# Optimization experiments

Measured on AMD Instinct MI355X. Metric: run time of the kernel, lower is better.

The kernel has to match this reference:

```python
import jax, jax.numpy as jnp
import numpy as np

STRIDES = (2, 2, 2, 2)
ALPHA = 1.0
NEG_SLOPE = 0.1


def _conv1d(h, w, b, stride):
    # h: (N, C, L), w: (O, I, K) -> (N, O, L_out), VALID padding
    out = jax.lax.conv_general_dilated(
        h, w, window_strides=(stride,), padding='VALID',
        dimension_numbers=('NCH', 'OIH', 'NCH'))
    return out + b[None, :, None]


def setup_inputs() -> dict:
    key = jax.random.key(0)
    ks = jax.random.split(key, 10)
    N, C, L = 256, 128, 1024
    k_sizes = (15, 12, 7, 4)
    inp = {'x': jax.random.normal(ks[0], (N, C, L), dtype=jnp.float32)}
    for i, k in enumerate(k_sizes):
        fan_in = C * k
        scale = 1.0 / np.sqrt(fan_in).astype(np.float32)
        inp[f'w{i+1}'] = jax.random.normal(ks[1 + 2 * i], (C, C, k), dtype=jnp.float32) * scale
        inp[f'b{i+1}'] = jax.random.normal(ks[2 + 2 * i], (C,), dtype=jnp.float32) * 0.01
    D = C * 59  # flattened encoder output: 1024->505->247->121->59
    inp['centers'] = jax.random.normal(ks[9], (64, D), dtype=jnp.float32)
    return inp


def reference(x, w1, b1, w2, b2, w3, b3, w4, b4, centers):
    ws = [(w1, b1), (w2, b2), (w3, b3), (w4, b4)]
    h = x
    for i, ((w, b), s) in enumerate(zip(ws, STRIDES)):
        h = _conv1d(h, w, b, s)
        if i != len(ws) - 1:
            h = jnp.where(h > 0, h, NEG_SLOPE * h)  # LeakyReLU(0.1)
    z = h.reshape(h.shape[0], -1)  # (N, D)
    # squared distances via norm expansion: ||z||^2 + ||c||^2 - 2 z.c
    d2 = (jnp.sum(z * z, axis=1, keepdims=True)
          + jnp.sum(centers * centers, axis=1)[None, :]
          - 2.0 * z @ centers.T)  # (N, K)
    q = 1.0 / (1.0 + d2 / ALPHA)
    q = q ** ((ALPHA + 1.0) / 2.0)
    q = q / jnp.sum(q, axis=1, keepdims=True)
    return q
```

## Files before the change

### kernel.cpp

```cpp
#include <hip/hip_runtime.h>

typedef __bf16 bf16;
typedef __bf16 bf16x4 __attribute__((ext_vector_type(4)));
typedef __bf16 bf16x8 __attribute__((ext_vector_type(8)));
typedef float f32x4 __attribute__((ext_vector_type(4)));

#define CCH 128

__global__ void k_prep_wall(const float* __restrict__ w1, const float* __restrict__ w2,
                            const float* __restrict__ w3, const float* __restrict__ w4,
                            bf16* __restrict__ o1, bf16* __restrict__ o2,
                            bf16* __restrict__ o3, bf16* __restrict__ o4) {
    int idx = blockIdx.x * 256 + threadIdx.x;
    const float* src; bf16* dst; int Kw; int r = idx;
    if (r < 15 * 16384) { src = w1; dst = o1; Kw = 15; }
    else if ((r -= 15 * 16384) < 12 * 16384) { src = w2; dst = o2; Kw = 12; }
    else if ((r -= 12 * 16384) < 7 * 16384) { src = w3; dst = o3; Kw = 7; }
    else if ((r -= 7 * 16384) < 4 * 16384) { src = w4; dst = o4; Kw = 4; }
    else return;
    int e = r & 7, lane = (r >> 3) & 63, og = (r >> 9) & 7, c = (r >> 12) & 3, kt = r >> 14;
    int o = og * 16 + (lane & 15);
    int i = c * 32 + (lane >> 4) * 8 + e;
    dst[r] = (bf16)src[(o * 128 + i) * Kw + kt];
}

__global__ void k_prep_c(const float* __restrict__ c, bf16* __restrict__ cbp,
                         float* __restrict__ cc) {
    int k = blockIdx.x;
    int tid = threadIdx.x;
    float s = 0.f;
    for (int idx = tid; idx < 64 * 128; idx += 256) {
        int l = idx >> 7;
        int o = idx & 127;
        float v = (l < 59) ? c[k * 7552 + o * 59 + l] : 0.f;
        bf16 b = (bf16)v;
        cbp[(size_t)k * 64 * 128 + idx] = b;
        float fv = (float)b;
        s += fv * fv;
    }
    __shared__ float red[256];
    red[tid] = s;
    __syncthreads();
    for (int st = 128; st > 0; st >>= 1) {
        if (tid < st) red[tid] += red[tid + st];
        __syncthreads();
    }
    if (tid == 0) cc[k] = red[0];
}

__global__ __launch_bounds__(256, 4) void k_conv1(
    const float* __restrict__ x, const bf16* __restrict__ wTp,
    const float* __restrict__ bias, bf16* __restrict__ out) {
    constexpr int KW = 15, LT = 128, PH = 2, OUT_ROWS = 512;
    constexpr int P = (LT - 1) * 2 + KW;
    constexpr int CPP = 64;
    constexpr int KC = 2;
    constexpr int RS = CPP;
    constexpr int NLT = LT / 16;
    constexpr int ESE = 136;
    constexpr int SMELE = (P * RS > LT * ESE) ? P * RS : LT * ESE;
    constexpr int NJ = KW * KC;
    __shared__ __align__(16) bf16 smem[SMELE];

    const int n = blockIdx.y;
    const int l0 = blockIdx.x * LT;
    const int p0 = l0 * 2;
    const int tid = threadIdx.x;
    const int wid = tid >> 6;
    const int lane = tid & 63;
    const int quad = lane >> 4;
    const int l15 = lane & 15;
    const int og0 = wid * 2;

    f32x4 acc[2][NLT];
#pragma unroll
    for (int a = 0; a < 2; ++a)
#pragma unroll
        for (int b = 0; b < NLT; ++b) acc[a][b] = (f32x4){0.f, 0.f, 0.f, 0.f};

    bf16x8 afr[2][2];
    const bf16* wbase = wTp + (size_t)lane * 8;
    afr[0][0] = *(const bf16x8*)(wbase + ((size_t)(og0 + 0) << 9));
    afr[0][1] = *(const bf16x8*)(wbase + ((size_t)(og0 + 1) << 9));

    const int cst = tid >> 2;
    const int qw = tid & 3;

#pragma unroll 1
    for (int ph = 0; ph < PH; ++ph) {
        if (ph) __syncthreads();

        const float* bch = x + ((size_t)(n * 128 + ph * 64 + cst)) * 1024;
#pragma unroll 4
        for (int it = 0; it < 17; ++it) {
            int pp = it * 16 + qw * 4;
            int gp = p0 + pp;
            f32x4 t;
            if (gp + 3 < 1024) {
                t = *(const f32x4*)(bch + gp);
            } else {
#pragma unroll
                for (int e = 0; e < 4; ++e) t[e] = (gp + e < 1024) ? bch[gp + e] : 0.f;
            }
#pragma unroll
            for (int e = 0; e < 4; ++e) {
                int ppe = pp + e;
                int sc8 = (((cst >> 3) ^ ((ppe >> 1) & 7)) << 3) | (cst & 7);
                smem[ppe * RS + sc8] = (bf16)t[e];
            }
        }
        __syncthreads();

#pragma unroll 2
        for (int j = 0; j < NJ; ++j) {
            int nj = j + 1, nph = ph;
            if (nj == NJ) { nj = 0; ++nph; }
            if (nph < PH) {
                int kt1 = nj >> 1;
                int c1 = (nj & (KC - 1)) + nph * KC;
                const bf16* wp = wbase + ((size_t)((kt1 * 4 + c1) * 8 + og0) << 9);
                afr[(j + 1) & 1][0] = *(const bf16x8*)(wp);
                afr[(j + 1) & 1][1] = *(const bf16x8*)(wp + 512);
            }
            const int kt = j >> 1;
            const int c16l = (j & (KC - 1)) * 4 + quad;
#pragma unroll
            for (int lt = 0; lt < NLT; ++lt) {
                int p = (lt * 16 + l15) * 2 + kt;
                int sc = c16l ^ ((p >> 1) & 7);
                bf16x8 bfr = *(const bf16x8*)(smem + p * RS + sc * 8);
                acc[0][lt] = __builtin_amdgcn_mfma_f32_16x16x32_bf16(
                    afr[j & 1][0], bfr, acc[0][lt], 0, 0, 0);
                acc[1][lt] = __builtin_amdgcn_mfma_f32_16x16x32_bf16(
                    afr[j & 1][1], bfr, acc[1][lt], 0, 0, 0);
            }
        }
    }

    __syncthreads();
#pragma unroll
    for (int ot = 0; ot < 2; ++ot) {
        const int o0 = wid * 32 + ot * 16 + quad * 4;
        const f32x4 bv = *(const f32x4*)(bias + o0);
#pragma unroll
        for (int lt = 0; lt < NLT; ++lt) {
            const int l = lt * 16 + l15;
            bf16x4 pk;
#pragma unroll
            for (int r = 0; r < 4; ++r) {
                float v = acc[ot][lt][r] + bv[r];
                v = (v > 0.f) ? v : 0.1f * v;
                pk[r] = (bf16)v;
            }
            *(bf16x4*)(smem + l * ESE + o0) = pk;
        }
    }
    __syncthreads();
    constexpr int SNIT = LT * 16 / 256;
    bf16* op = out + ((size_t)n * OUT_ROWS + l0) * CCH;
#pragma unroll
    for (int it = 0; it < SNIT; ++it) {
        int u = tid + it * 256;
        int l = u >> 4;
        int g = u & 15;
        *(bf16x8*)(op + l * CCH + g * 8) = *(const bf16x8*)(smem + l * ESE + g * 8);
    }
}

template <int KW, int IN_CAP, int OUT_ROWS, int LT, int PH, bool ACT>
__global__ __launch_bounds__(256, 4) void k_conv(
    const bf16* __restrict__ in_, const bf16* __restrict__ wTp,
    const float* __restrict__ bias, bf16* __restrict__ out) {
    constexpr int P = (LT - 1) * 2 + KW;
    constexpr int CPP = 128 / PH;
    constexpr int KC = CPP / 32;
    constexpr int C16N = CPP / 8;
    constexpr int RS = CPP;
    constexpr int KCL = (KC == 4) ? 2 : 1;
    constexpr int NLT = LT / 16;
    constexpr int ESE = 136;
    constexpr int SMELE = (P * RS > LT * ESE) ? P * RS : LT * ESE;
    constexpr int NJ = KW * KC;
    __shared__ __align__(16) bf16 smem[SMELE];

    const int n = blockIdx.y;
    const int l0 = blockIdx.x * LT;
    const int p0 = l0 * 2;
    const int tid = threadIdx.x;
    const int wid = tid >> 6;
    const int lane = tid & 63;
    const int quad = lane >> 4;
    const int l15 = lane & 15;
    const int og0 = wid * 2;

    f32x4 acc[2][NLT];
#pragma unroll
    for (int a = 0; a < 2; ++a)
#pragma unroll
        for (int b = 0; b < NLT; ++b) acc[a][b] = (f32x4){0.f, 0.f, 0.f, 0.f};

    bf16x8 afr[2][2];
    const bf16* wbase = wTp + (size_t)lane * 8;

    afr[0][0] = *(const bf16x8*)(wbase + ((size_t)(og0 + 0) << 9));
    afr[0][1] = *(const bf16x8*)(wbase + ((size_t)(og0 + 1) << 9));

#pragma unroll 1
    for (int ph = 0; ph < PH; ++ph) {
        if (ph) __syncthreads();

        constexpr int UNITS = P * C16N;
        constexpr int NIT = (UNITS + 255) / 256;
        const bf16* base = in_ + ((size_t)n * IN_CAP + p0) * CCH + ph * CPP;
#pragma unroll
        for (int it = 0; it < NIT; ++it) {
            int u = tid + it * 256;
            if ((UNITS & 255) == 0 || u < UNITS) {
                int p = u >> ((C16N == 16) ? 4 : 3);
                int c = u & (C16N - 1);
                bf16x8 t = *(const bf16x8*)(base + (size_t)p * CCH + c * 8);
                int sc = (PH == 2) ? (c ^ ((p >> 1) & 7))
                                   : ((c & 8) | ((c & 7) ^ ((p >> 1) & 7)));
                *(bf16x8*)(smem + p * RS + sc * 8) = t;
            }
        }
        __syncthreads();

#pragma unroll 2
        for (int j = 0; j < NJ; ++j) {
            int nj = j + 1, nph = ph;
            if (nj == NJ) { nj = 0; ++nph; }
            if (nph < PH) {
                int kt1 = nj >> KCL;
                int c1 = (nj & (KC - 1)) + nph * KC;
                const bf16* wp = wbase + ((size_t)((kt1 * 4 + c1) * 8 + og0) << 9);
                afr[(j + 1) & 1][0] = *(const bf16x8*)(wp);
                afr[(j + 1) & 1][1] = *(const bf16x8*)(wp + 512);
            }
            const int kt = j >> KCL;
            const int c16l = (j & (KC - 1)) * 4 + quad;
#pragma unroll
            for (int lt = 0; lt < NLT; ++lt) {
                int p = (lt * 16 + l15) * 2 + kt;
                int sc = (PH == 2) ? (c16l ^ ((p >> 1) & 7))
                                   : ((c16l & 8) | ((c16l & 7) ^ ((p >> 1) & 7)));
                bf16x8 bfr = *(const bf16x8*)(smem + p * RS + sc * 8);
                acc[0][lt] = __builtin_amdgcn_mfma_f32_16x16x32_bf16(
                    afr[j & 1][0], bfr, acc[0][lt], 0, 0, 0);
                acc[1][lt] = __builtin_amdgcn_mfma_f32_16x16x32_bf16(
                    afr[j & 1][1], bfr, acc[1][lt], 0, 0, 0);
            }
        }
    }

    __syncthreads();
#pragma unroll
    for (int ot = 0; ot < 2; ++ot) {
        const int o0 = wid * 32 + ot * 16 + quad * 4;
        const f32x4 bv = *(const f32x4*)(bias + o0);
#pragma unroll
        for (int lt = 0; lt < NLT; ++lt) {
            const int l = lt * 16 + l15;
            bf16x4 pk;
#pragma unroll
            for (int r = 0; r < 4; ++r) {
                float v = acc[ot][lt][r] + bv[r];
                if (ACT) v = (v > 0.f) ? v : 0.1f * v;
                pk[r] = (bf16)v;
            }
            *(bf16x4*)(smem + l * ESE + o0) = pk;
        }
    }
    __syncthreads();
    constexpr int SNIT = LT * 16 / 256;
    bf16* op = out + ((size_t)n * OUT_ROWS + l0) * CCH;
#pragma unroll
    for (int it = 0; it < SNIT; ++it) {
        int u = tid + it * 256;
        int l = u >> 4;
        int g = u & 15;
        *(bf16x8*)(op + l * CCH + g * 8) = *(const bf16x8*)(smem + l * ESE + g * 8);
    }
}

__global__ __launch_bounds__(512, 1) void k_conv4_dist(
    const bf16* __restrict__ in_, const bf16* __restrict__ wTp,
    const float* __restrict__ bias, const bf16* __restrict__ cbp,
    const float* __restrict__ cc, float* __restrict__ out) {
    constexpr int P = 130, NJ = 16;
    constexpr int ESE = 136;
    __shared__ __align__(16) bf16 smem[P * 128];
    __shared__ __align__(16) bf16 zmem[64 * ESE];
    __shared__ float d2s[64];

    const int n = blockIdx.x;
    const int tid = threadIdx.x;
    const int wid = tid >> 6;
    const int lane = tid & 63;
    const int quad = lane >> 4;
    const int l15 = lane & 15;

    f32x4 acc[4];
#pragma unroll
    for (int b = 0; b < 4; ++b) acc[b] = (f32x4){0.f, 0.f, 0.f, 0.f};

    bf16x8 afr[2];
    const bf16* wbase = wTp + (size_t)lane * 8;
    afr[0] = *(const bf16x8*)(wbase + ((size_t)wid << 9));

    {
        constexpr int UNITS = P * 16;
        const bf16* base = in_ + (size_t)n * 128 * CCH;
#pragma unroll
        for (int it = 0; it < 5; ++it) {
            int u = tid + it * 512;
            if (u < UNITS) {
                int p = u >> 4;
                int c = u & 15;
                bf16x8 t = *(const bf16x8*)(base + (size_t)p * CCH + c * 8);
                int sc = (c & 8) | ((c & 7) ^ ((p >> 1) & 7));
                *(bf16x8*)(smem + p * 128 + sc * 8) = t;
            }
        }
    }
    __syncthreads();

#pragma unroll 2
    for (int j = 0; j < NJ; ++j) {
        if (j + 1 < NJ) {
            int kt1 = (j + 1) >> 2;
            int c1 = (j + 1) & 3;
            afr[(j + 1) & 1] =
                *(const bf16x8*)(wbase + ((size_t)((kt1 * 4 + c1) * 8 + wid) << 9));
        }
        const int kt = j >> 2;
        const int c16l = (j & 3) * 4 + quad;
#pragma unroll
        for (int lt = 0; lt < 4; ++lt) {
            int p = (lt * 16 + l15) * 2 + kt;
            int sc = (c16l & 8) | ((c16l & 7) ^ ((p >> 1) & 7));
            bf16x8 bfr = *(const bf16x8*)(smem + p * 128 + sc * 8);
            acc[lt] = __builtin_amdgcn_mfma_f32_16x16x32_bf16(afr[j & 1], bfr, acc[lt], 0, 0, 0);
        }
    }

    {
        const int o0 = wid * 16 + quad * 4;
        const f32x4 bv = *(const f32x4*)(bias + o0);
#pragma unroll
        for (int lt = 0; lt < 4; ++lt) {
            const int l = lt * 16 + l15;
            bf16x4 pk;
#pragma unroll
            for (int r = 0; r < 4; ++r) {
                float v = acc[lt][r] + bv[r];
                pk[r] = (l < 59) ? (bf16)v : (bf16)0.f;
            }
            *(bf16x4*)(zmem + l * ESE + o0) = pk;
        }
    }
    __syncthreads();

#pragma unroll 1
    for (int cp = 0; cp < 8; ++cp) {
        const int kc = cp * 8 + wid;
        const bf16* cr = cbp + (size_t)kc * 8192;
        float t = 0.f;
#pragma unroll
        for (int it = 0; it < 16; ++it) {
            int ci = it * 64 + lane;
            int l = ci >> 4;
            int g = ci & 15;
            bf16x8 cv = *(const bf16x8*)(cr + ci * 8);
            bf16x8 zv = *(const bf16x8*)(zmem + l * ESE + g * 8);
#pragma unroll
            for (int e = 0; e < 8; ++e) {
                float zf = (float)zv[e];
                t += zf * (zf - 2.f * (float)cv[e]);
            }
        }
#pragma unroll
        for (int o = 32; o > 0; o >>= 1) t += __shfl_xor(t, o);
        if (lane == 0) d2s[kc] = t + cc[kc];
    }
    __syncthreads();
    if (tid < 64) {
        float q = 1.f / (1.f + d2s[tid]);
        float tot = q;
#pragma unroll
        for (int o = 32; o > 0; o >>= 1) tot += __shfl_xor(tot, o);
        out[n * 64 + tid] = q / tot;
    }
}

extern "C" void kernel_launch(void* const* d_in, const int* in_sizes, int n_in,
                              void* d_out, int out_size, void* d_ws, size_t ws_size,
                              hipStream_t stream) {
    (void)in_sizes; (void)n_in; (void)out_size; (void)ws_size;
    const float* x   = (const float*)d_in[0];
    const float* w1  = (const float*)d_in[1];
    const float* b1  = (const float*)d_in[2];
    const float* w2  = (const float*)d_in[3];
    const float* b2  = (const float*)d_in[4];
    const float* w3  = (const float*)d_in[5];
    const float* b3  = (const float*)d_in[6];
    const float* w4  = (const float*)d_in[7];
    const float* b4  = (const float*)d_in[8];
    const float* cen = (const float*)d_in[9];
    float* out = (float*)d_out;

    char* ws = (char*)d_ws;
    size_t off = 0;
    auto alloc = [&](size_t bytes) -> void* {
        void* p = ws + off;
        off += (bytes + 255) & ~(size_t)255;
        return p;
    };
    bf16* wT1 = (bf16*)alloc((size_t)15 * 16384 * sizeof(bf16));
    bf16* wT2 = (bf16*)alloc((size_t)12 * 16384 * sizeof(bf16));
    bf16* wT3 = (bf16*)alloc((size_t)7 * 16384 * sizeof(bf16));
    bf16* wT4 = (bf16*)alloc((size_t)4 * 16384 * sizeof(bf16));
    bf16* cbp = (bf16*)alloc((size_t)64 * 64 * 128 * sizeof(bf16));
    float* cc = (float*)alloc(64 * sizeof(float));
    bf16* h1  = (bf16*)alloc((size_t)256 * 512 * 128 * sizeof(bf16));
    bf16* h2  = (bf16*)alloc((size_t)256 * 256 * 128 * sizeof(bf16));
    bf16* h3  = h1;
    (void)alloc((size_t)1 << 20);

    k_prep_wall<<<(38 * 16384 + 255) / 256, 256, 0, stream>>>(w1, w2, w3, w4, wT1, wT2, wT3, wT4);
    k_prep_c<<<64, 256, 0, stream>>>(cen, cbp, cc);

    k_conv1<<<dim3(4, 256), 256, 0, stream>>>(x, wT1, b1, h1);
    k_conv<12, 512, 256, 64, 1, true>
        <<<dim3(4, 256), 256, 0, stream>>>(h1, wT2, b2, h2);
    k_conv<7, 256, 128, 32, 1, true>
        <<<dim3(4, 256), 256, 0, stream>>>(h2, wT3, b3, h3);
    k_conv4_dist<<<256, 512, 0, stream>>>(h3, wT4, b4, cbp, cc, out);
}
```

Before: 342.4 us.

## Retile conv warps to 64 out-channels by half positions for B-fragment reuse

Each wave in the conv kernels now covers 4 output-channel tiles (half the channels) over half the position tiles, instead of 2 channel tiles over all positions. Every LDS B-fragment read now feeds 4 MFMAs rather than 2, cutting shared-memory read traffic per MFMA. In exchange each wave loads twice as many weight fragments from global/L2 per step and holds more A registers. conv1's launch bounds drop from 4 to 3 waves per SIMD to make room for those registers.

```diff
diff --git a/kernel.cpp b/kernel.cpp
--- a/kernel.cpp
+++ b/kernel.cpp
@@ -48,15 +48,14 @@
     if (tid == 0) cc[k] = red[0];
 }
 
-__global__ __launch_bounds__(256, 4) void k_conv1(
+__global__ __launch_bounds__(256, 3) void k_conv1(
     const float* __restrict__ x, const bf16* __restrict__ wTp,
     const float* __restrict__ bias, bf16* __restrict__ out) {
     constexpr int KW = 15, LT = 128, PH = 2, OUT_ROWS = 512;
     constexpr int P = (LT - 1) * 2 + KW;
-    constexpr int CPP = 64;
     constexpr int KC = 2;
-    constexpr int RS = CPP;
-    constexpr int NLT = LT / 16;
+    constexpr int RS = 64;
+    constexpr int NLTW = LT / 32;
     constexpr int ESE = 136;
     constexpr int SMELE = (P * RS > LT * ESE) ? P * RS : LT * ESE;
     constexpr int NJ = KW * KC;
@@ -70,18 +69,20 @@
     const int lane = tid & 63;
     const int quad = lane >> 4;
     const int l15 = lane & 15;
-    const int og0 = wid * 2;
-
-    f32x4 acc[2][NLT];
-#pragma unroll
-    for (int a = 0; a < 2; ++a)
-#pragma unroll
-        for (int b = 0; b < NLT; ++b) acc[a][b] = (f32x4){0.f, 0.f, 0.f, 0.f};
-
-    bf16x8 afr[2][2];
-    const bf16* wbase = wTp + (size_t)lane * 8;
-    afr[0][0] = *(const bf16x8*)(wbase + ((size_t)(og0 + 0) << 9));
-    afr[0][1] = *(const bf16x8*)(wbase + ((size_t)(og0 + 1) << 9));
+    const int oh = wid & 1;
+    const int posbase = (wid >> 1) * (LT / 2);
+
+    f32x4 acc[4][NLTW];
+#pragma unroll
+    for (int a = 0; a < 4; ++a)
+#pragma unroll
+        for (int b = 0; b < NLTW; ++b) acc[a][b] = (f32x4){0.f, 0.f, 0.f, 0.f};
+
+    bf16x8 afr[2][4];
+    const bf16* wbase = wTp + (size_t)lane * 8 + ((size_t)(oh * 4) << 9);
+#pragma unroll
+    for (int a = 0; a < 4; ++a)
+        afr[0][a] = *(const bf16x8*)(wbase + ((size_t)a << 9));
 
     const int cst = tid >> 2;
     const int qw = tid & 3;
@@ -118,37 +119,38 @@
             if (nph < PH) {
                 int kt1 = nj >> 1;
                 int c1 = (nj & (KC - 1)) + nph * KC;
-                const bf16* wp = wbase + ((size_t)((kt1 * 4 + c1) * 8 + og0) << 9);
-                afr[(j + 1) & 1][0] = *(const bf16x8*)(wp);
-                afr[(j + 1) & 1][1] = *(const bf16x8*)(wp + 512);
+                const bf16* wp = wbase + ((size_t)((kt1 * 4 + c1) * 8) << 9);
+#pragma unroll
+                for (int a = 0; a < 4; ++a)
+                    afr[(j + 1) & 1][a] = *(const bf16x8*)(wp + ((size_t)a << 9));
             }
             const int kt = j >> 1;
             const int c16l = (j & (KC - 1)) * 4 + quad;
 #pragma unroll
-            for (int lt = 0; lt < NLT; ++lt) {
-                int p = (lt * 16 + l15) * 2 + kt;
+            for (int lt = 0; lt < NLTW; ++lt) {
+                int p = (posbase + lt * 16 + l15) * 2 + kt;
                 int sc = c16l ^ ((p >> 1) & 7);
                 bf16x8 bfr = *(const bf16x8*)(smem + p * RS + sc * 8);
-                acc[0][lt] = __builtin_amdgcn_mfma_f32_16x16x32_bf16(
-                    afr[j & 1][0], bfr, acc[0][lt], 0, 0, 0);
-                acc[1][lt] = __builtin_amdgcn_mfma_f32_16x16x32_bf16(
-                    afr[j & 1][1], bfr, acc[1][lt], 0, 0, 0);
-            }
-        }
-    }
-
-    __syncthreads();
-#pragma unroll
-    for (int ot = 0; ot < 2; ++ot) {
-        const int o0 = wid * 32 + ot * 16 + quad * 4;
+#pragma unroll
+                for (int a = 0; a < 4; ++a)
+                    acc[a][lt] = __builtin_amdgcn_mfma_f32_16x16x32_bf16(
+                        afr[j & 1][a], bfr, acc[a][lt], 0, 0, 0);
+            }
+        }
+    }
+
+    __syncthreads();
+#pragma unroll
+    for (int a = 0; a < 4; ++a) {
+        const int o0 = (oh * 4 + a) * 16 + quad * 4;
         const f32x4 bv = *(const f32x4*)(bias + o0);
 #pragma unroll
-        for (int lt = 0; lt < NLT; ++lt) {
-            const int l = lt * 16 + l15;
+        for (int lt = 0; lt < NLTW; ++lt) {
+            const int l = posbase + lt * 16 + l15;
             bf16x4 pk;
 #pragma unroll
             for (int r = 0; r < 4; ++r) {
-                float v = acc[ot][lt][r] + bv[r];
+                float v = acc[a][lt][r] + bv[r];
                 v = (v > 0.f) ? v : 0.1f * v;
                 pk[r] = (bf16)v;
             }
@@ -177,7 +179,7 @@
     constexpr int C16N = CPP / 8;
     constexpr int RS = CPP;
     constexpr int KCL = (KC == 4) ? 2 : 1;
-    constexpr int NLT = LT / 16;
+    constexpr int NLTW = LT / 32;
     constexpr int ESE = 136;
     constexpr int SMELE = (P * RS > LT * ESE) ? P * RS : LT * ESE;
     constexpr int NJ = KW * KC;
@@ -191,19 +193,20 @@
     const int lane = tid & 63;
     const int quad = lane >> 4;
     const int l15 = lane & 15;
-    const int og0 = wid * 2;
-
-    f32x4 acc[2][NLT];
-#pragma unroll
-    for (int a = 0; a < 2; ++a)
-#pragma unroll
-        for (int b = 0; b < NLT; ++b) acc[a][b] = (f32x4){0.f, 0.f, 0.f, 0.f};
-
-    bf16x8 afr[2][2];
-    const bf16* wbase = wTp + (size_t)lane * 8;
-
-    afr[0][0] = *(const bf16x8*)(wbase + ((size_t)(og0 + 0) << 9));
-    afr[0][1] = *(const bf16x8*)(wbase + ((size_t)(og0 + 1) << 9));
+    const int oh = wid & 1;
+    const int posbase = (wid >> 1) * (LT / 2);
+
+    f32x4 acc[4][NLTW];
+#pragma unroll
+    for (int a = 0; a < 4; ++a)
+#pragma unroll
+        for (int b = 0; b < NLTW; ++b) acc[a][b] = (f32x4){0.f, 0.f, 0.f, 0.f};
+
+    bf16x8 afr[2][4];
+    const bf16* wbase = wTp + (size_t)lane * 8 + ((size_t)(oh * 4) << 9);
+#pragma unroll
+    for (int a = 0; a < 4; ++a)
+        afr[0][a] = *(const bf16x8*)(wbase + ((size_t)a << 9));
 
 #pragma unroll 1
     for (int ph = 0; ph < PH; ++ph) {
@@ -233,38 +236,39 @@
             if (nph < PH) {
                 int kt1 = nj >> KCL;
                 int c1 = (nj & (KC - 1)) + nph * KC;
-                const bf16* wp = wbase + ((size_t)((kt1 * 4 + c1) * 8 + og0) << 9);
-                afr[(j + 1) & 1][0] = *(const bf16x8*)(wp);
-                afr[(j + 1) & 1][1] = *(const bf16x8*)(wp + 512);
+                const bf16* wp = wbase + ((size_t)((kt1 * 4 + c1) * 8) << 9);
+#pragma unroll
+                for (int a = 0; a < 4; ++a)
+                    afr[(j + 1) & 1][a] = *(const bf16x8*)(wp + ((size_t)a << 9));
             }
             const int kt = j >> KCL;
             const int c16l = (j & (KC - 1)) * 4 + quad;
 #pragma unroll
-            for (int lt = 0; lt < NLT; ++lt) {
-                int p = (lt * 16 + l15) * 2 + kt;
+            for (int lt = 0; lt < NLTW; ++lt) {
+                int p = (posbase + lt * 16 + l15) * 2 + kt;
                 int sc = (PH == 2) ? (c16l ^ ((p >> 1) & 7))
                                    : ((c16l & 8) | ((c16l & 7) ^ ((p >> 1) & 7)));
                 bf16x8 bfr = *(const bf16x8*)(smem + p * RS + sc * 8);
-                acc[0][lt] = __builtin_amdgcn_mfma_f32_16x16x32_bf16(
-                    afr[j & 1][0], bfr, acc[0][lt], 0, 0, 0);
-                acc[1][lt] = __builtin_amdgcn_mfma_f32_16x16x32_bf16(
-                    afr[j & 1][1], bfr, acc[1][lt], 0, 0, 0);
-            }
-        }
-    }
-
-    __syncthreads();
-#pragma unroll
-    for (int ot = 0; ot < 2; ++ot) {
-        const int o0 = wid * 32 + ot * 16 + quad * 4;
+#pragma unroll
+                for (int a = 0; a < 4; ++a)
+                    acc[a][lt] = __builtin_amdgcn_mfma_f32_16x16x32_bf16(
+                        afr[j & 1][a], bfr, acc[a][lt], 0, 0, 0);
+            }
+        }
+    }
+
+    __syncthreads();
+#pragma unroll
+    for (int a = 0; a < 4; ++a) {
+        const int o0 = (oh * 4 + a) * 16 + quad * 4;
         const f32x4 bv = *(const f32x4*)(bias + o0);
 #pragma unroll
-        for (int lt = 0; lt < NLT; ++lt) {
-            const int l = lt * 16 + l15;
+        for (int lt = 0; lt < NLTW; ++lt) {
+            const int l = posbase + lt * 16 + l15;
             bf16x4 pk;
 #pragma unroll
             for (int r = 0; r < 4; ++r) {
-                float v = acc[ot][lt][r] + bv[r];
+                float v = acc[a][lt][r] + bv[r];
                 if (ACT) v = (v > 0.f) ? v : 0.1f * v;
                 pk[r] = (bf16)v;
             }
@@ -299,14 +303,18 @@
     const int lane = tid & 63;
     const int quad = lane >> 4;
     const int l15 = lane & 15;
+    const int oh = wid & 1;
+    const int pq = wid >> 1;
 
     f32x4 acc[4];
 #pragma unroll
     for (int b = 0; b < 4; ++b) acc[b] = (f32x4){0.f, 0.f, 0.f, 0.f};
 
-    bf16x8 afr[2];
-    const bf16* wbase = wTp + (size_t)lane * 8;
-    afr[0] = *(const bf16x8*)(wbase + ((size_t)wid << 9));
+    bf16x8 afr[2][4];
+    const bf16* wbase = wTp + (size_t)lane * 8 + ((size_t)(oh * 4) << 9);
+#pragma unroll
+    for (int a = 0; a < 4; ++a)
+        afr[0][a] = *(const bf16x8*)(wbase + ((size_t)a << 9));
 
     {
         constexpr int UNITS = P * 16;
@@ -330,30 +338,31 @@
         if (j + 1 < NJ) {
             int kt1 = (j + 1) >> 2;
             int c1 = (j + 1) & 3;
-            afr[(j + 1) & 1] =
-                *(const bf16x8*)(wbase + ((size_t)((kt1 * 4 + c1) * 8 + wid) << 9));
+            const bf16* wp = wbase + ((size_t)((kt1 * 4 + c1) * 8) << 9);
+#pragma unroll
+            for (int a = 0; a < 4; ++a)
+                afr[(j + 1) & 1][a] = *(const bf16x8*)(wp + ((size_t)a << 9));
         }
         const int kt = j >> 2;
         const int c16l = (j & 3) * 4 + quad;
-#pragma unroll
-        for (int lt = 0; lt < 4; ++lt) {
-            int p = (lt * 16 + l15) * 2 + kt;
-            int sc = (c16l & 8) | ((c16l & 7) ^ ((p >> 1) & 7));
-            bf16x8 bfr = *(const bf16x8*)(smem + p * 128 + sc * 8);
-            acc[lt] = __builtin_amdgcn_mfma_f32_16x16x32_bf16(afr[j & 1], bfr, acc[lt], 0, 0, 0);
-        }
+        int p = (pq * 16 + l15) * 2 + kt;
+        int sc = (c16l & 8) | ((c16l & 7) ^ ((p >> 1) & 7));
+        bf16x8 bfr = *(const bf16x8*)(smem + p * 128 + sc * 8);
+#pragma unroll
+        for (int a = 0; a < 4; ++a)
+            acc[a] = __builtin_amdgcn_mfma_f32_16x16x32_bf16(afr[j & 1][a], bfr, acc[a], 0, 0, 0);
     }
 
     {
-        const int o0 = wid * 16 + quad * 4;
-        const f32x4 bv = *(const f32x4*)(bias + o0);
-#pragma unroll
-        for (int lt = 0; lt < 4; ++lt) {
-            const int l = lt * 16 + l15;
+        const int l = pq * 16 + l15;
+#pragma unroll
+        for (int a = 0; a < 4; ++a) {
+            const int o0 = (oh * 4 + a) * 16 + quad * 4;
+            const f32x4 bv = *(const f32x4*)(bias + o0);
             bf16x4 pk;
 #pragma unroll
             for (int r = 0; r < 4; ++r) {
-                float v = acc[lt][r] + bv[r];
+                float v = acc[a][r] + bv[r];
                 pk[r] = (l < 59) ? (bf16)v : (bf16)0.f;
             }
             *(bf16x4*)(zmem + l * ESE + o0) = pk;
```

Result: slower. 380.8 us (+11.2%).

## Fuse conv2, conv3, conv4 and distance head into one per-sample LDS kernel

Applied to the files above, without the earlier changes.

Replaces the separate conv2 and conv3 launches and the conv4+distance kernel with one kernel per batch sample. That kernel keeps the conv2 and conv3 activations in LDS (about 135 KB) and only streams h1 from global memory. It also merges the two prep kernels into one launch. The aim is to remove the global round-trips of h2/h3 and several launch overheads. In exchange, the grid drops to 256 blocks of 512 threads with one block per CU, so occupancy is low and there is less parallelism.

```diff
diff --git a/kernel.cpp b/kernel.cpp
--- a/kernel.cpp
+++ b/kernel.cpp
@@ -7,45 +7,46 @@
 
 #define CCH 128
 
-__global__ void k_prep_wall(const float* __restrict__ w1, const float* __restrict__ w2,
-                            const float* __restrict__ w3, const float* __restrict__ w4,
-                            bf16* __restrict__ o1, bf16* __restrict__ o2,
-                            bf16* __restrict__ o3, bf16* __restrict__ o4) {
-    int idx = blockIdx.x * 256 + threadIdx.x;
-    const float* src; bf16* dst; int Kw; int r = idx;
-    if (r < 15 * 16384) { src = w1; dst = o1; Kw = 15; }
-    else if ((r -= 15 * 16384) < 12 * 16384) { src = w2; dst = o2; Kw = 12; }
-    else if ((r -= 12 * 16384) < 7 * 16384) { src = w3; dst = o3; Kw = 7; }
-    else if ((r -= 7 * 16384) < 4 * 16384) { src = w4; dst = o4; Kw = 4; }
-    else return;
-    int e = r & 7, lane = (r >> 3) & 63, og = (r >> 9) & 7, c = (r >> 12) & 3, kt = r >> 14;
-    int o = og * 16 + (lane & 15);
-    int i = c * 32 + (lane >> 4) * 8 + e;
-    dst[r] = (bf16)src[(o * 128 + i) * Kw + kt];
-}
-
-__global__ void k_prep_c(const float* __restrict__ c, bf16* __restrict__ cbp,
-                         float* __restrict__ cc) {
-    int k = blockIdx.x;
+__global__ void k_prep_all(const float* __restrict__ w1, const float* __restrict__ w2,
+                           const float* __restrict__ w3, const float* __restrict__ w4,
+                           const float* __restrict__ cen,
+                           bf16* __restrict__ o1, bf16* __restrict__ o2,
+                           bf16* __restrict__ o3, bf16* __restrict__ o4,
+                           bf16* __restrict__ cbp, float* __restrict__ cc) {
+    __shared__ float red[256];
     int tid = threadIdx.x;
-    float s = 0.f;
-    for (int idx = tid; idx < 64 * 128; idx += 256) {
-        int l = idx >> 7;
-        int o = idx & 127;
-        float v = (l < 59) ? c[k * 7552 + o * 59 + l] : 0.f;
-        bf16 b = (bf16)v;
-        cbp[(size_t)k * 64 * 128 + idx] = b;
-        float fv = (float)b;
-        s += fv * fv;
-    }
-    __shared__ float red[256];
-    red[tid] = s;
-    __syncthreads();
-    for (int st = 128; st > 0; st >>= 1) {
-        if (tid < st) red[tid] += red[tid + st];
+    if (blockIdx.x < 2432) {
+        int idx = blockIdx.x * 256 + tid;
+        const float* src; bf16* dst; int Kw; int r = idx;
+        if (r < 15 * 16384) { src = w1; dst = o1; Kw = 15; }
+        else if ((r -= 15 * 16384) < 12 * 16384) { src = w2; dst = o2; Kw = 12; }
+        else if ((r -= 12 * 16384) < 7 * 16384) { src = w3; dst = o3; Kw = 7; }
+        else if ((r -= 7 * 16384) < 4 * 16384) { src = w4; dst = o4; Kw = 4; }
+        else return;
+        int e = r & 7, lane = (r >> 3) & 63, og = (r >> 9) & 7, c = (r >> 12) & 3, kt = r >> 14;
+        int o = og * 16 + (lane & 15);
+        int i = c * 32 + (lane >> 4) * 8 + e;
+        dst[r] = (bf16)src[(o * 128 + i) * Kw + kt];
+    } else {
+        int k = blockIdx.x - 2432;
+        float s = 0.f;
+        for (int idx = tid; idx < 64 * 128; idx += 256) {
+            int l = idx >> 7;
+            int o = idx & 127;
+            float v = (l < 59) ? cen[k * 7552 + o * 59 + l] : 0.f;
+            bf16 b = (bf16)v;
+            cbp[(size_t)k * 64 * 128 + idx] = b;
+            float fv = (float)b;
+            s += fv * fv;
+        }
+        red[tid] = s;
         __syncthreads();
-    }
-    if (tid == 0) cc[k] = red[0];
+        for (int st = 128; st > 0; st >>= 1) {
+            if (tid < st) red[tid] += red[tid + st];
+            __syncthreads();
+        }
+        if (tid == 0) cc[k] = red[0];
+    }
 }
 
 __global__ __launch_bounds__(256, 4) void k_conv1(
@@ -53,9 +54,8 @@
     const float* __restrict__ bias, bf16* __restrict__ out) {
     constexpr int KW = 15, LT = 128, PH = 2, OUT_ROWS = 512;
     constexpr int P = (LT - 1) * 2 + KW;
-    constexpr int CPP = 64;
     constexpr int KC = 2;
-    constexpr int RS = CPP;
+    constexpr int RS = 64;
     constexpr int NLT = LT / 16;
     constexpr int ESE = 136;
     constexpr int SMELE = (P * RS > LT * ESE) ? P * RS : LT * ESE;
@@ -167,131 +167,18 @@
     }
 }
 
-template <int KW, int IN_CAP, int OUT_ROWS, int LT, int PH, bool ACT>
-__global__ __launch_bounds__(256, 4) void k_conv(
-    const bf16* __restrict__ in_, const bf16* __restrict__ wTp,
-    const float* __restrict__ bias, bf16* __restrict__ out) {
-    constexpr int P = (LT - 1) * 2 + KW;
-    constexpr int CPP = 128 / PH;
-    constexpr int KC = CPP / 32;
-    constexpr int C16N = CPP / 8;
-    constexpr int RS = CPP;
-    constexpr int KCL = (KC == 4) ? 2 : 1;
-    constexpr int NLT = LT / 16;
-    constexpr int ESE = 136;
-    constexpr int SMELE = (P * RS > LT * ESE) ? P * RS : LT * ESE;
-    constexpr int NJ = KW * KC;
-    __shared__ __align__(16) bf16 smem[SMELE];
-
-    const int n = blockIdx.y;
-    const int l0 = blockIdx.x * LT;
-    const int p0 = l0 * 2;
-    const int tid = threadIdx.x;
-    const int wid = tid >> 6;
-    const int lane = tid & 63;
-    const int quad = lane >> 4;
-    const int l15 = lane & 15;
-    const int og0 = wid * 2;
-
-    f32x4 acc[2][NLT];
-#pragma unroll
-    for (int a = 0; a < 2; ++a)
-#pragma unroll
-        for (int b = 0; b < NLT; ++b) acc[a][b] = (f32x4){0.f, 0.f, 0.f, 0.f};
-
-    bf16x8 afr[2][2];
-    const bf16* wbase = wTp + (size_t)lane * 8;
-
-    afr[0][0] = *(const bf16x8*)(wbase + ((size_t)(og0 + 0) << 9));
-    afr[0][1] = *(const bf16x8*)(wbase + ((size_t)(og0 + 1) << 9));
-
-#pragma unroll 1
-    for (int ph = 0; ph < PH; ++ph) {
-        if (ph) __syncthreads();
-
-        constexpr int UNITS = P * C16N;
-        constexpr int NIT = (UNITS + 255) / 256;
-        const bf16* base = in_ + ((size_t)n * IN_CAP + p0) * CCH + ph * CPP;
-#pragma unroll
-        for (int it = 0; it < NIT; ++it) {
-            int u = tid + it * 256;
-            if ((UNITS & 255) == 0 || u < UNITS) {
-                int p = u >> ((C16N == 16) ? 4 : 3);
-                int c = u & (C16N - 1);
-                bf16x8 t = *(const bf16x8*)(base + (size_t)p * CCH + c * 8);
-                int sc = (PH == 2) ? (c ^ ((p >> 1) & 7))
-                                   : ((c & 8) | ((c & 7) ^ ((p >> 1) & 7)));
-                *(bf16x8*)(smem + p * RS + sc * 8) = t;
-            }
-        }
-        __syncthreads();
-
-#pragma unroll 2
-        for (int j = 0; j < NJ; ++j) {
-            int nj = j + 1, nph = ph;
-            if (nj == NJ) { nj = 0; ++nph; }
-            if (nph < PH) {
-                int kt1 = nj >> KCL;
-                int c1 = (nj & (KC - 1)) + nph * KC;
-                const bf16* wp = wbase + ((size_t)((kt1 * 4 + c1) * 8 + og0) << 9);
-                afr[(j + 1) & 1][0] = *(const bf16x8*)(wp);
-                afr[(j + 1) & 1][1] = *(const bf16x8*)(wp + 512);
-            }
-            const int kt = j >> KCL;
-            const int c16l = (j & (KC - 1)) * 4 + quad;
-#pragma unroll
-            for (int lt = 0; lt < NLT; ++lt) {
-                int p = (lt * 16 + l15) * 2 + kt;
-                int sc = (PH == 2) ? (c16l ^ ((p >> 1) & 7))
-                                   : ((c16l & 8) | ((c16l & 7) ^ ((p >> 1) & 7)));
-                bf16x8 bfr = *(const bf16x8*)(smem + p * RS + sc * 8);
-                acc[0][lt] = __builtin_amdgcn_mfma_f32_16x16x32_bf16(
-                    afr[j & 1][0], bfr, acc[0][lt], 0, 0, 0);
-                acc[1][lt] = __builtin_amdgcn_mfma_f32_16x16x32_bf16(
-                    afr[j & 1][1], bfr, acc[1][lt], 0, 0, 0);
-            }
-        }
-    }
-
-    __syncthreads();
-#pragma unroll
-    for (int ot = 0; ot < 2; ++ot) {
-        const int o0 = wid * 32 + ot * 16 + quad * 4;
-        const f32x4 bv = *(const f32x4*)(bias + o0);
-#pragma unroll
-        for (int lt = 0; lt < NLT; ++lt) {
-            const int l = lt * 16 + l15;
-            bf16x4 pk;
-#pragma unroll
-            for (int r = 0; r < 4; ++r) {
-                float v = acc[ot][lt][r] + bv[r];
-                if (ACT) v = (v > 0.f) ? v : 0.1f * v;
-                pk[r] = (bf16)v;
-            }
-            *(bf16x4*)(smem + l * ESE + o0) = pk;
-        }
-    }
-    __syncthreads();
-    constexpr int SNIT = LT * 16 / 256;
-    bf16* op = out + ((size_t)n * OUT_ROWS + l0) * CCH;
-#pragma unroll
-    for (int it = 0; it < SNIT; ++it) {
-        int u = tid + it * 256;
-        int l = u >> 4;
-        int g = u & 15;
-        *(bf16x8*)(op + l * CCH + g * 8) = *(const bf16x8*)(smem + l * ESE + g * 8);
-    }
-}
-
-__global__ __launch_bounds__(512, 1) void k_conv4_dist(
-    const bf16* __restrict__ in_, const bf16* __restrict__ wTp,
-    const float* __restrict__ bias, const bf16* __restrict__ cbp,
+__global__ __launch_bounds__(512, 1) void k_fused234(
+    const bf16* __restrict__ h1g, const bf16* __restrict__ wT2,
+    const bf16* __restrict__ wT3, const bf16* __restrict__ wT4,
+    const float* __restrict__ b2, const float* __restrict__ b3,
+    const float* __restrict__ b4, const bf16* __restrict__ cbp,
     const float* __restrict__ cc, float* __restrict__ out) {
-    constexpr int P = 130, NJ = 16;
-    constexpr int ESE = 136;
-    __shared__ __align__(16) bf16 smem[P * 128];
-    __shared__ __align__(16) bf16 zmem[64 * ESE];
+    __shared__ __align__(16) bf16 lds[34048 + 33536];
     __shared__ float d2s[64];
+    bf16* sbuf = lds;
+    bf16* h2   = lds + 34048;
+    bf16* h3   = lds;
+    bf16* zmem = lds + 16640;
 
     const int n = blockIdx.x;
     const int tid = threadIdx.x;
@@ -300,53 +187,170 @@
     const int quad = lane >> 4;
     const int l15 = lane & 15;
 
-    f32x4 acc[4];
-#pragma unroll
-    for (int b = 0; b < 4; ++b) acc[b] = (f32x4){0.f, 0.f, 0.f, 0.f};
-
-    bf16x8 afr[2];
-    const bf16* wbase = wTp + (size_t)lane * 8;
-    afr[0] = *(const bf16x8*)(wbase + ((size_t)wid << 9));
+    if (tid < 96) *(f32x4*)(h2 + 256 * 128 + tid * 8) = (f32x4){0.f, 0.f, 0.f, 0.f};
 
     {
-        constexpr int UNITS = P * 16;
-        const bf16* base = in_ + (size_t)n * 128 * CCH;
-#pragma unroll
-        for (int it = 0; it < 5; ++it) {
-            int u = tid + it * 512;
-            if (u < UNITS) {
-                int p = u >> 4;
-                int c = u & 15;
-                bf16x8 t = *(const bf16x8*)(base + (size_t)p * CCH + c * 8);
-                int sc = (c & 8) | ((c & 7) ^ ((p >> 1) & 7));
-                *(bf16x8*)(smem + p * 128 + sc * 8) = t;
+        const int w4 = wid & 3;
+        const int g = wid >> 2;
+        const int og0 = w4 * 2;
+        const bf16* w2base = wT2 + (size_t)lane * 8;
+        constexpr int NJ2 = 48;
+#pragma unroll 1
+        for (int s = 0; s < 2; ++s) {
+            if (s) __syncthreads();
+            {
+                const bf16* base = h1g + (size_t)n * 512 * 128;
+#pragma unroll
+                for (int it = 0; it < 9; ++it) {
+                    int u = tid + it * 512;
+                    if (u < 266 * 16) {
+                        int p = u >> 4, c = u & 15;
+                        int prow = s * 256 + p; if (prow > 511) prow = 511;
+                        bf16x8 t = *(const bf16x8*)(base + (size_t)prow * 128 + c * 8);
+                        int sc = (c & 8) | ((c & 7) ^ ((p >> 1) & 7));
+                        *(bf16x8*)(sbuf + p * 128 + sc * 8) = t;
+                    }
+                }
+            }
+            __syncthreads();
+
+            f32x4 acc[2][4];
+#pragma unroll
+            for (int a = 0; a < 2; ++a)
+#pragma unroll
+                for (int b = 0; b < 4; ++b) acc[a][b] = (f32x4){0.f, 0.f, 0.f, 0.f};
+            bf16x8 afr[2][2];
+            afr[0][0] = *(const bf16x8*)(w2base + ((size_t)og0 << 9));
+            afr[0][1] = *(const bf16x8*)(w2base + ((size_t)(og0 + 1) << 9));
+#pragma unroll 2
+            for (int j = 0; j < NJ2; ++j) {
+                if (j + 1 < NJ2) {
+                    int kt1 = (j + 1) >> 2, c1 = (j + 1) & 3;
+                    const bf16* wp = w2base + ((size_t)((kt1 * 4 + c1) * 8 + og0) << 9);
+                    afr[(j + 1) & 1][0] = *(const bf16x8*)(wp);
+                    afr[(j + 1) & 1][1] = *(const bf16x8*)(wp + 512);
+                }
+                int kt = j >> 2;
+                int c16l = (j & 3) * 4 + quad;
+#pragma unroll
+                for (int lt = 0; lt < 4; ++lt) {
+                    int p = (g * 64 + lt * 16 + l15) * 2 + kt;
+                    int sc = (c16l & 8) | ((c16l & 7) ^ ((p >> 1) & 7));
+                    bf16x8 bfr = *(const bf16x8*)(sbuf + p * 128 + sc * 8);
+                    acc[0][lt] = __builtin_amdgcn_mfma_f32_16x16x32_bf16(
+                        afr[j & 1][0], bfr, acc[0][lt], 0, 0, 0);
+                    acc[1][lt] = __builtin_amdgcn_mfma_f32_16x16x32_bf16(
+                        afr[j & 1][1], bfr, acc[1][lt], 0, 0, 0);
+                }
+            }
+#pragma unroll
+            for (int ot = 0; ot < 2; ++ot) {
+                int o0 = (og0 + ot) * 16 + quad * 4;
+                f32x4 bv = *(const f32x4*)(b2 + o0);
+                int c = o0 >> 3;
+#pragma unroll
+                for (int lt = 0; lt < 4; ++lt) {
+                    int l = s * 128 + g * 64 + lt * 16 + l15;
+                    bf16x4 pk;
+#pragma unroll
+                    for (int r = 0; r < 4; ++r) {
+                        float v = acc[ot][lt][r] + bv[r];
+                        v = (v > 0.f) ? v : 0.1f * v;
+                        pk[r] = (bf16)v;
+                    }
+                    int sc = (c & 8) | ((c & 7) ^ ((l >> 1) & 7));
+                    *(bf16x4*)(h2 + l * 128 + sc * 8 + (o0 & 7)) = pk;
+                }
+            }
+            __syncthreads();
+        }
+    }
+
+    {
+        if (tid < 32) *(f32x4*)(h3 + 128 * 128 + tid * 8) = (f32x4){0.f, 0.f, 0.f, 0.f};
+        const int og0 = (wid & 3) * 2;
+        const int ph3 = wid >> 2;
+        const bf16* w3base = wT3 + (size_t)lane * 8;
+        constexpr int NJ3 = 28;
+        f32x4 acc[2][4];
+#pragma unroll
+        for (int a = 0; a < 2; ++a)
+#pragma unroll
+            for (int b = 0; b < 4; ++b) acc[a][b] = (f32x4){0.f, 0.f, 0.f, 0.f};
+        bf16x8 afr[2][2];
+        afr[0][0] = *(const bf16x8*)(w3base + ((size_t)og0 << 9));
+        afr[0][1] = *(const bf16x8*)(w3base + ((size_t)(og0 + 1) << 9));
+#pragma unroll 2
+        for (int j = 0; j < NJ3; ++j) {
+            if (j + 1 < NJ3) {
+                int kt1 = (j + 1) >> 2, c1 = (j + 1) & 3;
+                const bf16* wp = w3base + ((size_t)((kt1 * 4 + c1) * 8 + og0) << 9);
+                afr[(j + 1) & 1][0] = *(const bf16x8*)(wp);
+                afr[(j + 1) & 1][1] = *(const bf16x8*)(wp + 512);
+            }
+            int kt = j >> 2;
+            int c16l = (j & 3) * 4 + quad;
+#pragma unroll
+            for (int lt = 0; lt < 4; ++lt) {
+                int p = (ph3 * 64 + lt * 16 + l15) * 2 + kt;
+                int sc = (c16l & 8) | ((c16l & 7) ^ ((p >> 1) & 7));
+                bf16x8 bfr = *(const bf16x8*)(h2 + p * 128 + sc * 8);
+                acc[0][lt] = __builtin_amdgcn_mfma_f32_16x16x32_bf16(
+                    afr[j & 1][0], bfr, acc[0][lt], 0, 0, 0);
+                acc[1][lt] = __builtin_amdgcn_mfma_f32_16x16x32_bf16(
+                    afr[j & 1][1], bfr, acc[1][lt], 0, 0, 0);
+            }
+        }
+        __syncthreads();
+#pragma unroll
+        for (int ot = 0; ot < 2; ++ot) {
+            int o0 = (og0 + ot) * 16 + quad * 4;
+            f32x4 bv = *(const f32x4*)(b3 + o0);
+            int c = o0 >> 3;
+#pragma unroll
+            for (int lt = 0; lt < 4; ++lt) {
+                int l = ph3 * 64 + lt * 16 + l15;
+                bf16x4 pk;
+#pragma unroll
+                for (int r = 0; r < 4; ++r) {
+                    float v = acc[ot][lt][r] + bv[r];
+                    v = (v > 0.f) ? v : 0.1f * v;
+                    pk[r] = (bf16)v;
+                }
+                int sc = (c & 8) | ((c & 7) ^ ((l >> 1) & 7));
+                *(bf16x4*)(h3 + l * 128 + sc * 8 + (o0 & 7)) = pk;
             }
         }
     }
     __syncthreads();
 
+    {
+        f32x4 acc[4];
+#pragma unroll
+        for (int b = 0; b < 4; ++b) acc[b] = (f32x4){0.f, 0.f, 0.f, 0.f};
+        bf16x8 afr[2];
+        const bf16* w4base = wT4 + (size_t)lane * 8;
+        afr[0] = *(const bf16x8*)(w4base + ((size_t)wid << 9));
+        constexpr int NJ4 = 16;
 #pragma unroll 2
-    for (int j = 0; j < NJ; ++j) {
-        if (j + 1 < NJ) {
-            int kt1 = (j + 1) >> 2;
-            int c1 = (j + 1) & 3;
-            afr[(j + 1) & 1] =
-                *(const bf16x8*)(wbase + ((size_t)((kt1 * 4 + c1) * 8 + wid) << 9));
-        }
-        const int kt = j >> 2;
-        const int c16l = (j & 3) * 4 + quad;
-#pragma unroll
-        for (int lt = 0; lt < 4; ++lt) {
-            int p = (lt * 16 + l15) * 2 + kt;
-            int sc = (c16l & 8) | ((c16l & 7) ^ ((p >> 1) & 7));
-            bf16x8 bfr = *(const bf16x8*)(smem + p * 128 + sc * 8);
-            acc[lt] = __builtin_amdgcn_mfma_f32_16x16x32_bf16(afr[j & 1], bfr, acc[lt], 0, 0, 0);
-        }
-    }
-
-    {
+        for (int j = 0; j < NJ4; ++j) {
+            if (j + 1 < NJ4) {
+                int kt1 = (j + 1) >> 2, c1 = (j + 1) & 3;
+                afr[(j + 1) & 1] =
+                    *(const bf16x8*)(w4base + ((size_t)((kt1 * 4 + c1) * 8 + wid) << 9));
+            }
+            int kt = j >> 2;
+            int c16l = (j & 3) * 4 + quad;
+#pragma unroll
+            for (int lt = 0; lt < 4; ++lt) {
+                int p = (lt * 16 + l15) * 2 + kt;
+                int sc = (c16l & 8) | ((c16l & 7) ^ ((p >> 1) & 7));
+                bf16x8 bfr = *(const bf16x8*)(h3 + p * 128 + sc * 8);
+                acc[lt] = __builtin_amdgcn_mfma_f32_16x16x32_bf16(afr[j & 1], bfr, acc[lt], 0, 0, 0);
+            }
+        }
         const int o0 = wid * 16 + quad * 4;
-        const f32x4 bv = *(const f32x4*)(bias + o0);
+        const f32x4 bv = *(const f32x4*)(b4 + o0);
 #pragma unroll
         for (int lt = 0; lt < 4; ++lt) {
             const int l = lt * 16 + l15;
@@ -356,7 +360,7 @@
                 float v = acc[lt][r] + bv[r];
                 pk[r] = (l < 59) ? (bf16)v : (bf16)0.f;
             }
-            *(bf16x4*)(zmem + l * ESE + o0) = pk;
+            *(bf16x4*)(zmem + l * 136 + o0) = pk;
         }
     }
     __syncthreads();
@@ -372,7 +376,7 @@
             int l = ci >> 4;
             int g = ci & 15;
             bf16x8 cv = *(const bf16x8*)(cr + ci * 8);
-            bf16x8 zv = *(const bf16x8*)(zmem + l * ESE + g * 8);
+            bf16x8 zv = *(const bf16x8*)(zmem + l * 136 + g * 8);
 #pragma unroll
             for (int e = 0; e < 8; ++e) {
                 float zf = (float)zv[e];
@@ -423,17 +427,10 @@
     bf16* cbp = (bf16*)alloc((size_t)64 * 64 * 128 * sizeof(bf16));
     float* cc = (float*)alloc(64 * sizeof(float));
     bf16* h1  = (bf16*)alloc((size_t)256 * 512 * 128 * sizeof(bf16));
-    bf16* h2  = (bf16*)alloc((size_t)256 * 256 * 128 * sizeof(bf16));
-    bf16* h3  = h1;
     (void)alloc((size_t)1 << 20);
 
-    k_prep_wall<<<(38 * 16384 + 255) / 256, 256, 0, stream>>>(w1, w2, w3, w4, wT1, wT2, wT3, wT4);
-    k_prep_c<<<64, 256, 0, stream>>>(cen, cbp, cc);
-
+    k_prep_all<<<2432 + 64, 256, 0, stream>>>(w1, w2, w3, w4, cen,
+                                              wT1, wT2, wT3, wT4, cbp, cc);
     k_conv1<<<dim3(4, 256), 256, 0, stream>>>(x, wT1, b1, h1);
-    k_conv<12, 512, 256, 64, 1, true>
-        <<<dim3(4, 256), 256, 0, stream>>>(h1, wT2, b2, h2);
-    k_conv<7, 256, 128, 32, 1, true>
-        <<<dim3(4, 256), 256, 0, stream>>>(h2, wT3, b3, h3);
-    k_conv4_dist<<<256, 512, 0, stream>>>(h3, wT4, b4, cbp, cc, out);
+    k_fused234<<<256, 512, 0, stream>>>(h1, wT2, wT3, wT4, b2, b3, b4, cbp, cc, out);
 }
```

Result: faster. 312.4 us (-8.8%).
